# Kernel tuning notes

Hardware: AMD Instinct MI355X
Metric: run time of the kernel (lower is better)

## Reference

```python
import jax, jax.numpy as jnp
import numpy as np

NW, NT = 200000, 100000
DW, DT = 128, 64
HID, HEADS, OUT = 64, 2, 2
HC = HID * HEADS  # 128
E = 500000
NEG_SLOPE = 0.2


def setup_inputs() -> dict:
    key = jax.random.key(0)
    ks = iter(jax.random.split(key, 40))

    def nrm(shape, scale):
        return jax.random.normal(next(ks), shape, dtype=jnp.float32) * scale

    inp = {
        "x_wallet": nrm((NW, DW), 1.0),
        "x_token": nrm((NT, DT), 1.0),
        # per-node-type input projections Linear(in, hidden)
        "lin_w_W": nrm((DW, HID), 1.0 / np.sqrt(DW)),
        "lin_w_b": jnp.zeros((HID,), jnp.float32),
        "lin_t_W": nrm((DT, HID), 1.0 / np.sqrt(DT)),
        "lin_t_b": jnp.zeros((HID,), jnp.float32),
        # GAT layer 0: in=HID(64) -> H*C(128), stacked over 3 edge types
        "Wsrc0": nrm((3, HID, HC), 1.0 / np.sqrt(HID)),
        "Wdst0": nrm((3, HID, HC), 1.0 / np.sqrt(HID)),
        "atts0": nrm((3, HEADS, HID), 1.0 / np.sqrt(HID)),
        "attd0": nrm((3, HEADS, HID), 1.0 / np.sqrt(HID)),
        "b0": jnp.zeros((3, HC), jnp.float32),
        # GAT layer 1: in=H*C(128) -> H*C(128)
        "Wsrc1": nrm((3, HC, HC), 1.0 / np.sqrt(HC)),
        "Wdst1": nrm((3, HC, HC), 1.0 / np.sqrt(HC)),
        "atts1": nrm((3, HEADS, HID), 1.0 / np.sqrt(HID)),
        "attd1": nrm((3, HEADS, HID), 1.0 / np.sqrt(HID)),
        "b1": jnp.zeros((3, HC), jnp.float32),
        # classifiers Linear(H*C, out)
        "cls_w_W": nrm((HC, OUT), 1.0 / np.sqrt(HC)),
        "cls_w_b": jnp.zeros((OUT,), jnp.float32),
        "cls_t_W": nrm((HC, OUT), 1.0 / np.sqrt(HC)),
        "cls_t_b": jnp.zeros((OUT,), jnp.float32),
        # edge indices: [2, E] with row0 = src ids, row1 = dst ids
        "e_wt": jnp.stack([jax.random.randint(next(ks), (E,), 0, NW),
                            jax.random.randint(next(ks), (E,), 0, NT)]).astype(jnp.int64),
        "e_tw": jnp.stack([jax.random.randint(next(ks), (E,), 0, NT),
                            jax.random.randint(next(ks), (E,), 0, NW)]).astype(jnp.int64),
        "e_ww": jnp.stack([jax.random.randint(next(ks), (E,), 0, NW),
                            jax.random.randint(next(ks), (E,), 0, NW)]).astype(jnp.int64),
    }
    return inp


def gat_conv(x_src, x_dst, edge, Wsrc, Wdst, att_s, att_d, bias, n_dst):
    # bipartite GATConv: project, per-edge attention, segment softmax over dst, scatter-sum
    hs = (x_src @ Wsrc).reshape(-1, HEADS, HID)  # [Ns,H,C]
    hd = (x_dst @ Wdst).reshape(-1, HEADS, HID)  # [Nd,H,C]
    a_s = jnp.einsum("nhc,hc->nh", hs, att_s)    # [Ns,H]
    a_d = jnp.einsum("nhc,hc->nh", hd, att_d)    # [Nd,H]
    s, d = edge[0], edge[1]
    alpha = jax.nn.leaky_relu(a_s[s] + a_d[d], NEG_SLOPE)  # [E,H]
    m = jax.ops.segment_max(alpha, d, num_segments=n_dst)
    m = jnp.where(jnp.isfinite(m), m, 0.0)  # nodes with no in-edges
    ex = jnp.exp(alpha - m[d])
    den = jax.ops.segment_sum(ex, d, num_segments=n_dst)
    alpha = ex / (den[d] + 1e-16)
    out = jax.ops.segment_sum(alpha[:, :, None] * hs[s], d, num_segments=n_dst)  # [Nd,H,C]
    return out.reshape(n_dst, HC) + bias


def reference(x_wallet, x_token, lin_w_W, lin_w_b, lin_t_W, lin_t_b,
              Wsrc0, Wdst0, atts0, attd0, b0,
              Wsrc1, Wdst1, atts1, attd1, b1,
              cls_w_W, cls_w_b, cls_t_W, cls_t_b,
              e_wt, e_tw, e_ww):
    xw = x_wallet @ lin_w_W + lin_w_b
    xt = x_token @ lin_t_W + lin_t_b
    for Wsrc, Wdst, ats, atd, b in ((Wsrc0, Wdst0, atts0, attd0, b0),
                                     (Wsrc1, Wdst1, atts1, attd1, b1)):
        # edge type 0: wallet->token, 1: token->wallet, 2: wallet->wallet; HeteroConv aggr='sum'
        out_t = gat_conv(xw, xt, e_wt, Wsrc[0], Wdst[0], ats[0], atd[0], b[0], NT)
        out_w = (gat_conv(xt, xw, e_tw, Wsrc[1], Wdst[1], ats[1], atd[1], b[1], NW)
                 + gat_conv(xw, xw, e_ww, Wsrc[2], Wdst[2], ats[2], atd[2], b[2], NW))
        xw = jax.nn.elu(out_w)
        xt = jax.nn.elu(out_t)
    logits_w = xw @ cls_w_W + cls_w_b  # [NW,2]
    logits_t = xt @ cls_t_W + cls_t_b  # [NT,2]
    return jnp.concatenate([logits_w, logits_t], axis=0)  # [NW+NT,2]
```

## Files before the change

kernel.cpp:

```cpp
#include <hip/hip_runtime.h>
#include <stdint.h>

typedef unsigned short ushort_t;
typedef short s8v __attribute__((ext_vector_type(8)));
typedef float f4v __attribute__((ext_vector_type(4)));

#define NW 200000
#define NT 100000
#define EE 500000
#define NSEG (NT + NW + NW)

__device__ __forceinline__ float b2f(unsigned short u){
  union { unsigned int i; float f; } v; v.i = ((unsigned int)u) << 16; return v.f;
}
__device__ __forceinline__ unsigned short f2b(float f){
  unsigned int x = __float_as_uint(f);
  unsigned int r = x + 0x7fffu + ((x >> 16) & 1u);
  return (unsigned short)(r >> 16);
}
__device__ __forceinline__ float ldf(const void* p, long idx, int fm){
  return fm ? ((const float*)p)[idx] : b2f(((const ushort_t*)p)[idx]);
}

__global__ void detect_kern(const int* ewt, const int* etw, const int* eww,
                            const unsigned* xw_words, int* mode){
  if (threadIdx.x == 0 && blockIdx.x == 0){
    unsigned o = 0;
    for (int i = 0; i < 64; ++i)
      o |= (unsigned)ewt[2 * i + 1] | (unsigned)etw[2 * i + 1] | (unsigned)eww[2 * i + 1];
    mode[0] = (o == 0) ? 1 : 0;
    int viol = 0;
    for (int i = 0; i < 256; ++i){
      unsigned s = xw_words[i] & 0xffffu;
      unsigned e = (s >> 7) & 0xffu;
      if (!(s == 0u || s == 0x8000u || (e >= 90u && e <= 140u))) viol++;
    }
    mode[1] = (viol > 8) ? 1 : 0;
  }
}

struct TDesc { const void* src; ushort_t* dst; long ebase; int K; int N; };
struct TDesc8 { TDesc d[8]; };
__global__ void transpose8(TDesc8 td, const int* mode){
  int fm = mode[1];
  int mi = blockIdx.x >> 6;
  TDesc t = td.d[mi];
  int e = ((blockIdx.x & 63) << 8) + threadIdx.x;
  if (e < t.K * t.N){
    int k = e / t.N, n = e - k * t.N;
    t.dst[n * t.K + k] = f2b(ldf(t.src, t.ebase + e, fm));
  }
}

__global__ void uprep(const void* Wsrc0, const void* Wdst0, const void* atts0, const void* attd0,
                      const void* Wsrc1, const void* Wdst1, const void* atts1, const void* attd1,
                      float* Uw0, float* Ut0, float* Uw1, float* Ut1, const int* mode){
  int fm = mode[1];
  int id = blockIdx.x * 256 + threadIdx.x;
  if (id >= (64 + 128) * 12) return;
  int layer = (id >= 64 * 12);
  int rem = layer ? id - 64 * 12 : id;
  int K = layer ? 128 : 64;
  int k = rem / 12, j = rem % 12;
  const void* Ws = layer ? Wsrc1 : Wsrc0;
  const void* Wd = layer ? Wdst1 : Wdst0;
  const void* As = layer ? atts1 : atts0;
  const void* Ad = layer ? attd1 : attd0;
  int t, h; bool src;
  if (j < 8){ const int tt[8] = {0,0,2,2,1,1,2,2}; t = tt[j]; h = j & 1; src = (j < 4); }
  else { int jj = j - 8; t = (jj < 2) ? 1 : 0; h = jj & 1; src = (jj < 2); }
  const void* W = src ? Ws : Wd;
  const void* A = src ? As : Ad;
  float acc = 0.f;
  for (int c = 0; c < 64; ++c)
    acc += ldf(W, (long)(t * K + k) * 128 + h * 64 + c, fm) * ldf(A, t * 128 + h * 64 + c, fm);
  if (j < 8) (layer ? Uw1 : Uw0)[k * 8 + j] = acc;
  else       (layer ? Ut1 : Ut0)[k * 4 + (j - 8)] = acc;
}

__global__ void hist_kern(const int* ewt, const int* etw, const int* eww, const int* mode, int* deg){
  int i = blockIdx.x * 256 + threadIdx.x;
  if (i >= 3 * EE) return;
  int md = mode[0];
  int t = i / EE, e = i - t * EE;
  const int* ep = (t == 0) ? ewt : (t == 1) ? etw : eww;
  int d = md ? ep[2 * (EE + e)] : ep[EE + e];
  int base = (t == 0) ? 0 : (t == 1) ? NT : NT + NW;
  atomicAdd(&deg[base + d], 1);
}

__global__ __launch_bounds__(512) void scan1(const int* deg, int* excl, int* sums){
  __shared__ int pair[512];
  int t = threadIdx.x;
  int base = blockIdx.x * 1024;
  int i0 = base + 2 * t;
  int a = (i0 < NSEG) ? deg[i0] : 0;
  int b = (i0 + 1 < NSEG) ? deg[i0 + 1] : 0;
  int ps = a + b;
  pair[t] = ps;
  __syncthreads();
  for (int off = 1; off < 512; off <<= 1){
    int v = (t >= off) ? pair[t - off] : 0;
    __syncthreads();
    if (t >= off) pair[t] += v;
    __syncthreads();
  }
  int epair = pair[t] - ps;
  if (i0 < NSEG) excl[i0] = epair;
  if (i0 + 1 < NSEG) excl[i0 + 1] = epair + a;
  if (t == 511) sums[blockIdx.x] = pair[511];
}

__global__ __launch_bounds__(512) void scan2(int* sums, int nch){
  __shared__ int s[512];
  int t = threadIdx.x;
  int orig = (t < nch) ? sums[t] : 0;
  s[t] = orig;
  __syncthreads();
  for (int off = 1; off < 512; off <<= 1){
    int v = (t >= off) ? s[t - off] : 0;
    __syncthreads();
    if (t >= off) s[t] += v;
    __syncthreads();
  }
  if (t < nch) sums[t] = s[t] - orig;
}

__global__ void scan3(int* rowptr, int* cursor, const int* sums){
  int i = blockIdx.x * 256 + threadIdx.x;
  if (i < NSEG){
    int v = rowptr[i] + sums[i >> 10];
    rowptr[i] = v; cursor[i] = v;
  }
  if (i == 0) rowptr[NSEG] = 3 * EE;
}

__global__ void fill_kern(const int* ewt, const int* etw, const int* eww, const int* mode,
                          int* cursor, int* adj){
  int i = blockIdx.x * 256 + threadIdx.x;
  if (i >= 3 * EE) return;
  int md = mode[0];
  int t = i / EE, e = i - t * EE;
  const int* ep = (t == 0) ? ewt : (t == 1) ? etw : eww;
  int s = md ? ep[2 * e] : ep[e];
  int d = md ? ep[2 * (EE + e)] : ep[EE + e];
  int base = (t == 0) ? 0 : (t == 1) ? NT : NT + NW;
  int pos = atomicAdd(&cursor[base + d], 1);
  adj[pos] = s;
}

template<int K, int NC, bool BIAS, bool EXTA>
__global__ __launch_bounds__(256, 2) void gemm_kern(const void* __restrict__ A, const ushort_t* __restrict__ Bt,
    const void* __restrict__ bias, ushort_t* __restrict__ C, int M,
    const int* __restrict__ mode, int nchunk){
  constexpr int CT = NC / 16, KK = K / 32;
  int fm = EXTA ? mode[1] : 0;
  int tid = threadIdx.x, lane = tid & 63, wave = tid >> 6;
  int rl = lane & 15, kq = (lane >> 4) * 8;
  s8v bfrag[CT][KK];
#pragma unroll
  for (int ct = 0; ct < CT; ++ct)
#pragma unroll
    for (int kk = 0; kk < KK; ++kk)
      bfrag[ct][kk] = *(const s8v*)(Bt + (long)(ct * 16 + rl) * K + kk * 32 + kq);
  float biasv[CT];
  if (BIAS){
#pragma unroll
    for (int ct = 0; ct < CT; ++ct) biasv[ct] = ldf(bias, ct * 16 + rl, fm);
  }
  for (int chunk = blockIdx.x; chunk < nchunk; chunk += gridDim.x){
    long m0 = (long)chunk * 128 + wave * 32;
    f4v acc[2][CT];
#pragma unroll
    for (int rt = 0; rt < 2; ++rt)
#pragma unroll
      for (int ct = 0; ct < CT; ++ct) acc[rt][ct] = (f4v){0.f, 0.f, 0.f, 0.f};
#pragma unroll
    for (int rt = 0; rt < 2; ++rt){
      long row = m0 + rt * 16 + rl;
      bool ok = row < (long)M;
#pragma unroll
      for (int kk = 0; kk < KK; ++kk){
        s8v a = (s8v){0,0,0,0,0,0,0,0};
        if (ok){
          long e = row * K + kk * 32 + kq;
          if (EXTA && fm){
            const float* p = (const float*)A + e;
            uint4 lo = *(const uint4*)p;
            uint4 hi = *(const uint4*)(p + 4);
            union { s8v v; unsigned u[4]; } t;
            t.u[0] = (unsigned)f2b(__uint_as_float(lo.x)) | ((unsigned)f2b(__uint_as_float(lo.y)) << 16);
            t.u[1] = (unsigned)f2b(__uint_as_float(lo.z)) | ((unsigned)f2b(__uint_as_float(lo.w)) << 16);
            t.u[2] = (unsigned)f2b(__uint_as_float(hi.x)) | ((unsigned)f2b(__uint_as_float(hi.y)) << 16);
            t.u[3] = (unsigned)f2b(__uint_as_float(hi.z)) | ((unsigned)f2b(__uint_as_float(hi.w)) << 16);
            a = t.v;
          } else {
            a = *(const s8v*)((const ushort_t*)A + e);
          }
        }
#pragma unroll
        for (int ct = 0; ct < CT; ++ct)
          acc[rt][ct] = __builtin_amdgcn_mfma_f32_16x16x32_bf16(a, bfrag[ct][kk], acc[rt][ct], 0, 0, 0);
      }
    }
#pragma unroll
    for (int rt = 0; rt < 2; ++rt){
      long rbase = (long)chunk * 128 + wave * 32 + rt * 16 + (lane >> 4) * 4;
#pragma unroll
      for (int ct = 0; ct < CT; ++ct){
#pragma unroll
        for (int r = 0; r < 4; ++r){
          long gm = rbase + r;
          if (gm < (long)M){
            float v = acc[rt][ct][r];
            if (BIAS) v += biasv[ct];
            C[gm * NC + ct * 16 + rl] = f2b(v);
          }
        }
      }
    }
  }
}

template<int K, int NCOL>
__global__ __launch_bounds__(256) void a_kern(const ushort_t* __restrict__ x, const float* __restrict__ U,
                                              float* __restrict__ out, int N){
  int n = blockIdx.x * 256 + threadIdx.x;
  if (n >= N) return;
  float acc[NCOL];
#pragma unroll
  for (int j = 0; j < NCOL; ++j) acc[j] = 0.f;
  const ushort_t* xr = x + (long)n * K;
#pragma unroll
  for (int k8 = 0; k8 < K / 8; ++k8){
    uint4 v = *(const uint4*)(xr + k8 * 8);
    unsigned uu[4] = {v.x, v.y, v.z, v.w};
#pragma unroll
    for (int i = 0; i < 4; ++i){
      float f0 = b2f((unsigned short)(uu[i] & 0xffffu));
      float f1 = b2f((unsigned short)(uu[i] >> 16));
      const float* Ur = U + (k8 * 8 + i * 2) * NCOL;
#pragma unroll
      for (int j = 0; j < NCOL; ++j) acc[j] += f0 * Ur[j] + f1 * Ur[NCOL + j];
    }
  }
  float* o = out + (long)n * (2 * NCOL);
#pragma unroll
  for (int q = 0; q < NCOL / 2; ++q){
    f4v t = {__expf(acc[2 * q]), __expf(0.2f * acc[2 * q]),
             __expf(acc[2 * q + 1]), __expf(0.2f * acc[2 * q + 1])};
    *(f4v*)(o + q * 4) = t;
  }
}

__device__ __forceinline__ void round_load(const int* __restrict__ adj,
    const float* __restrict__ psrc, int sstr, int j, int cnt,
    const ushort_t* __restrict__ hb, float2 (&pq)[8], unsigned (&h)[8]){
#pragma unroll
  for (int i = 0; i < 8; ++i){
    if (i < cnt){
      int s = adj[j + i];
      pq[i] = *(const float2*)(psrc + (long)s * sstr);
      h[i] = *(const unsigned*)(hb + (long)s * 128);
    }
  }
}

__device__ __forceinline__ void round_acc(int cnt, float pd, float qd,
    const float2 (&pq)[8], const unsigned (&h)[8], float& n0, float& n1, float& den){
#pragma unroll
  for (int i = 0; i < 8; ++i){
    if (i < cnt){
      float t = pq[i].x * pd, u = pq[i].y * qd;
      float w = t > 1.f ? t : u;
      den += w;
      n0 += w * b2f((unsigned short)(h[i] & 0xffffu));
      n1 += w * b2f((unsigned short)(h[i] >> 16));
    }
  }
}

template<bool FINAL>
__global__ __launch_bounds__(256) void agg_all(const int* __restrict__ rowptr, const int* __restrict__ adj,
    const float* __restrict__ aw, const float* __restrict__ at,
    const ushort_t* __restrict__ hs0, const ushort_t* __restrict__ hs1, const ushort_t* __restrict__ hs2,
    const void* __restrict__ bsrc, ushort_t* __restrict__ xt_out, ushort_t* __restrict__ xw_out,
    const void* __restrict__ clsWw, const void* __restrict__ clsbw,
    const void* __restrict__ clsWt, const void* __restrict__ clsbt,
    void* __restrict__ dout, const int* __restrict__ mode){
  int fm = mode[1];
  int wv = __builtin_amdgcn_readfirstlane(threadIdx.x >> 6);
  int lane = threadIdx.x & 63;
  int hh = lane >> 5;
  int c0 = lane << 1;
  int bid = blockIdx.x;
  const int TB = NT / 4;
  bool is_tok = bid < TB;
  float o0, o1;
  int d;
  if (is_tok){
    d = bid * 4 + wv;
    float2 dq = *(const float2*)(at + (long)d * 8 + 4 + hh * 2);
    const float* ps = aw + hh * 2;
    const ushort_t* hb = hs0 + c0;
    int beg = rowptr[d], end = rowptr[d + 1];
    float n0 = 0.f, n1 = 0.f, den = 0.f;
    for (int j = beg; j < end; j += 8){
      int cnt = min(end - j, 8);
      float2 pq[8]; unsigned h[8];
      round_load(adj, ps, 16, j, cnt, hb, pq, h);
      round_acc(cnt, dq.x, dq.y, pq, h, n0, n1, den);
    }
    float inv = 1.f / (den + 1e-16f);
    o0 = n0 * inv + ldf(bsrc, c0, fm);
    o1 = n1 * inv + ldf(bsrc, c0 + 1, fm);
  } else {
    d = (bid - TB) * 4 + wv;
    const float* awd = aw + (long)d * 16;
    float2 dq1 = *(const float2*)(awd + 8 + hh * 2);
    float2 dq2 = *(const float2*)(awd + 12 + hh * 2);
    const float* ps1 = at + hh * 2;
    const float* ps2 = aw + 4 + hh * 2;
    const ushort_t* hb1 = hs1 + c0;
    const ushort_t* hb2 = hs2 + c0;
    int s1 = NT + d, s2 = NT + NW + d;
    int b1 = rowptr[s1], e1 = rowptr[s1 + 1];
    int b2 = rowptr[s2], e2 = rowptr[s2 + 1];
    int c1 = min(e1 - b1, 8), c2 = min(e2 - b2, 8);
    float n10 = 0.f, n11 = 0.f, den1 = 0.f;
    float n20 = 0.f, n21 = 0.f, den2 = 0.f;
    {
      float2 pq1[8], pq2[8]; unsigned h1[8], h2[8];
      if (c1 > 0) round_load(adj, ps1, 8, b1, c1, hb1, pq1, h1);
      if (c2 > 0) round_load(adj, ps2, 16, b2, c2, hb2, pq2, h2);
      if (c1 > 0) round_acc(c1, dq1.x, dq1.y, pq1, h1, n10, n11, den1);
      if (c2 > 0) round_acc(c2, dq2.x, dq2.y, pq2, h2, n20, n21, den2);
    }
    for (int j = b1 + 8; j < e1; j += 8){
      int cnt = min(e1 - j, 8);
      float2 pq[8]; unsigned h[8];
      round_load(adj, ps1, 8, j, cnt, hb1, pq, h);
      round_acc(cnt, dq1.x, dq1.y, pq, h, n10, n11, den1);
    }
    for (int j = b2 + 8; j < e2; j += 8){
      int cnt = min(e2 - j, 8);
      float2 pq[8]; unsigned h[8];
      round_load(adj, ps2, 16, j, cnt, hb2, pq, h);
      round_acc(cnt, dq2.x, dq2.y, pq, h, n20, n21, den2);
    }
    float i1v = 1.f / (den1 + 1e-16f), i2v = 1.f / (den2 + 1e-16f);
    o0 = n10 * i1v + n20 * i2v + ldf(bsrc, 128 + c0, fm)     + ldf(bsrc, 256 + c0, fm);
    o1 = n11 * i1v + n21 * i2v + ldf(bsrc, 128 + c0 + 1, fm) + ldf(bsrc, 256 + c0 + 1, fm);
  }
  o0 = o0 > 0.f ? o0 : __expf(o0) - 1.f;
  o1 = o1 > 0.f ? o1 : __expf(o1) - 1.f;
  if (!FINAL){
    ushort_t* out = is_tok ? xt_out : xw_out;
    unsigned pack = (unsigned)f2b(o0) | ((unsigned)f2b(o1) << 16);
    *(unsigned*)(out + (long)d * 128 + c0) = pack;
  } else {
    const void* W = is_tok ? clsWt : clsWw;
    const void* b = is_tok ? clsbt : clsbw;
    float w00 = ldf(W, 4 * lane + 0, fm), w01 = ldf(W, 4 * lane + 1, fm);
    float w10 = ldf(W, 4 * lane + 2, fm), w11 = ldf(W, 4 * lane + 3, fm);
    float p0 = o0 * w00 + o1 * w10;
    float p1 = o0 * w01 + o1 * w11;
#pragma unroll
    for (int off = 32; off > 0; off >>= 1){ p0 += __shfl_xor(p0, off, 64); p1 += __shfl_xor(p1, off, 64); }
    if (lane == 0){
      long g = is_tok ? (long)NW + d : (long)d;
      float r0 = p0 + ldf(b, 0, fm);
      float r1 = p1 + ldf(b, 1, fm);
      if (fm){ ((float*)dout)[g * 2] = r0; ((float*)dout)[g * 2 + 1] = r1; }
      else { ((ushort_t*)dout)[g * 2] = f2b(r0); ((ushort_t*)dout)[g * 2 + 1] = f2b(r1); }
    }
  }
}

extern "C" void kernel_launch(void* const* d_in, const int* in_sizes, int n_in,
                              void* d_out, int out_size, void* d_ws, size_t ws_size,
                              hipStream_t stream){
  const void* x_wallet = d_in[0];
  const void* x_token  = d_in[1];
  const void* lin_w_W  = d_in[2];
  const void* lin_w_b  = d_in[3];
  const void* lin_t_W  = d_in[4];
  const void* lin_t_b  = d_in[5];
  const void* Wsrc0    = d_in[6];
  const void* Wdst0    = d_in[7];
  const void* atts0    = d_in[8];
  const void* attd0    = d_in[9];
  const void* b0       = d_in[10];
  const void* Wsrc1    = d_in[11];
  const void* Wdst1    = d_in[12];
  const void* atts1    = d_in[13];
  const void* attd1    = d_in[14];
  const void* b1       = d_in[15];
  const void* cls_w_W  = d_in[16];
  const void* cls_w_b  = d_in[17];
  const void* cls_t_W  = d_in[18];
  const void* cls_t_b  = d_in[19];
  const int* e_wt = (const int*)d_in[20];
  const int* e_tw = (const int*)d_in[21];
  const int* e_ww = (const int*)d_in[22];

  char* ws = (char*)d_ws;
  size_t off = 0;
  auto alloc = [&](size_t bytes) -> char* {
    char* p = ws + off; off += (bytes + 255) & ~(size_t)255; return p;
  };
  int* rowptr = (int*)alloc((size_t)(NSEG + 1) * 4);
  int* deg    = (int*)alloc((size_t)(NSEG + 1) * 4);
  int* adj    = (int*)alloc((size_t)3 * EE * 4);
  int* sums   = (int*)alloc(512 * 4);
  int* mode   = (int*)alloc(8);
  ushort_t* BtLw = (ushort_t*)alloc(64 * 128 * 2);
  ushort_t* BtLt = (ushort_t*)alloc(64 * 64 * 2);
  ushort_t* BtS0 = (ushort_t*)alloc(3 * 128 * 64 * 2);
  ushort_t* BtS1 = (ushort_t*)alloc(3 * 128 * 128 * 2);
  float* Uw0 = (float*)alloc(64 * 8 * 4);
  float* Ut0 = (float*)alloc(64 * 4 * 4);
  float* Uw1 = (float*)alloc(128 * 8 * 4);
  float* Ut1 = (float*)alloc(128 * 4 * 4);
  float* aw = (float*)alloc((size_t)NW * 16 * 4);
  float* at = (float*)alloc((size_t)NT * 8 * 4);
  ushort_t* hs0 = (ushort_t*)alloc((size_t)NW * 128 * 2);
  ushort_t* hs1 = (ushort_t*)alloc((size_t)NT * 128 * 2);
  ushort_t* hs2 = (ushort_t*)alloc((size_t)NW * 128 * 2);
  ushort_t* xbuf = (ushort_t*)alloc(((size_t)NW + NT) * 128 * 2);
  ushort_t* xw0 = xbuf;
  ushort_t* xt0 = xbuf + (size_t)NW * 64;
  ushort_t* xwB = xbuf;
  ushort_t* xtB = xbuf + (size_t)NW * 128;
  (void)in_sizes; (void)n_in;

  if (off > ws_size){
    hipMemsetAsync(d_out, 0, (size_t)out_size * 2, stream);
    return;
  }

  hipMemsetAsync(deg, 0, (size_t)NSEG * 4, stream);
  detect_kern<<<1, 64, 0, stream>>>(e_wt, e_tw, e_ww, (const unsigned*)x_wallet, mode);

  TDesc8 td;
  td.d[0] = { lin_w_W, BtLw, 0, 128, 64 };
  td.d[1] = { lin_t_W, BtLt, 0, 64, 64 };
  for (int t = 0; t < 3; ++t){
    td.d[2 + t] = { Wsrc0, BtS0 + t * 128 * 64,  (long)t * 64 * 128,  64,  128 };
    td.d[5 + t] = { Wsrc1, BtS1 + t * 128 * 128, (long)t * 128 * 128, 128, 128 };
  }
  transpose8<<<512, 256, 0, stream>>>(td, mode);
  uprep<<<9, 256, 0, stream>>>(Wsrc0, Wdst0, atts0, attd0, Wsrc1, Wdst1, atts1, attd1, Uw0, Ut0, Uw1, Ut1, mode);

  int egrid = (3 * EE + 255) / 256;
  hist_kern<<<egrid, 256, 0, stream>>>(e_wt, e_tw, e_ww, mode, deg);
  int nch = (NSEG + 1023) / 1024;
  scan1<<<nch, 512, 0, stream>>>(deg, rowptr, sums);
  scan2<<<1, 512, 0, stream>>>(sums, nch);
  scan3<<<(NSEG + 255) / 256, 256, 0, stream>>>(rowptr, deg, sums);
  fill_kern<<<egrid, 256, 0, stream>>>(e_wt, e_tw, e_ww, mode, deg, adj);

  const int G = 512;
  int ncW = (NW + 127) / 128, ncT = (NT + 127) / 128;
  int agrid = NT / 4 + NW / 4;

  gemm_kern<128, 64, true, true><<<G, 256, 0, stream>>>(x_wallet, BtLw, lin_w_b, xw0, NW, mode, ncW);
  gemm_kern<64, 64, true, true><<<G, 256, 0, stream>>>(x_token, BtLt, lin_t_b, xt0, NT, mode, ncT);

  a_kern<64, 8><<<(NW + 255) / 256, 256, 0, stream>>>(xw0, Uw0, aw, NW);
  a_kern<64, 4><<<(NT + 255) / 256, 256, 0, stream>>>(xt0, Ut0, at, NT);
  gemm_kern<64, 128, false, false><<<G, 256, 0, stream>>>(xw0, BtS0, nullptr, hs0, NW, mode, ncW);
  gemm_kern<64, 128, false, false><<<G, 256, 0, stream>>>(xt0, BtS0 + 128 * 64, nullptr, hs1, NT, mode, ncT);
  gemm_kern<64, 128, false, false><<<G, 256, 0, stream>>>(xw0, BtS0 + 2 * 128 * 64, nullptr, hs2, NW, mode, ncW);
  agg_all<false><<<agrid, 256, 0, stream>>>(rowptr, adj, aw, at, hs0, hs1, hs2, b0, xtB, xwB,
                                            nullptr, nullptr, nullptr, nullptr, nullptr, mode);

  a_kern<128, 8><<<(NW + 255) / 256, 256, 0, stream>>>(xwB, Uw1, aw, NW);
  a_kern<128, 4><<<(NT + 255) / 256, 256, 0, stream>>>(xtB, Ut1, at, NT);
  gemm_kern<128, 128, false, false><<<G, 256, 0, stream>>>(xwB, BtS1, nullptr, hs0, NW, mode, ncW);
  gemm_kern<128, 128, false, false><<<G, 256, 0, stream>>>(xtB, BtS1 + 128 * 128, nullptr, hs1, NT, mode, ncT);
  gemm_kern<128, 128, false, false><<<G, 256, 0, stream>>>(xwB, BtS1 + 2 * 128 * 128, nullptr, hs2, NW, mode, ncW);
  agg_all<true><<<agrid, 256, 0, stream>>>(rowptr, adj, aw, at, hs0, hs1, hs2, b1, nullptr, nullptr,
                                           cls_w_W, cls_w_b, cls_t_W, cls_t_b, d_out, mode);
}
```

Measured before the change: 934.5 us.

## Interleave attention source coefficients into padded feature rows and split aggregation kernels

Source-side attention exponentials are now stored inside each projected feature row, which is padded from 128 to 160 bf16, so the gather per edge reads one row region instead of two separate arrays. Destination coefficients go to compact per-node arrays. The fused aggregation kernel is split into separate token and wallet kernels. The token kernel is launched right after its projection GEMM, so it can run before the other projections are computed. The cost is about 25% more bytes per feature row written by the GEMMs, and the rows lose 256-byte alignment.

```diff
diff --git a/kernel.cpp b/kernel.cpp
--- a/kernel.cpp
+++ b/kernel.cpp
@@ -9,6 +9,7 @@
 #define NT 100000
 #define EE 500000
 #define NSEG (NT + NW + NW)
+#define HRS 160
 
 __device__ __forceinline__ float b2f(unsigned short u){
   union { unsigned int i; float f; } v; v.i = ((unsigned int)u) << 16; return v.f;
@@ -149,7 +150,7 @@
   adj[pos] = s;
 }
 
-template<int K, int NC, bool BIAS, bool EXTA>
+template<int K, int NC, int RS, bool BIAS, bool EXTA>
 __global__ __launch_bounds__(256, 2) void gemm_kern(const void* __restrict__ A, const ushort_t* __restrict__ Bt,
     const void* __restrict__ bias, ushort_t* __restrict__ C, int M,
     const int* __restrict__ mode, int nchunk){
@@ -214,7 +215,7 @@
           if (gm < (long)M){
             float v = acc[rt][ct][r];
             if (BIAS) v += biasv[ct];
-            C[gm * NC + ct * 16 + rl] = f2b(v);
+            C[gm * RS + ct * 16 + rl] = f2b(v);
           }
         }
       }
@@ -222,9 +223,10 @@
   }
 }
 
-template<int K, int NCOL>
+template<int K, bool WAL>
 __global__ __launch_bounds__(256) void a_kern(const ushort_t* __restrict__ x, const float* __restrict__ U,
-                                              float* __restrict__ out, int N){
+    float* __restrict__ dpq, ushort_t* __restrict__ hsA, ushort_t* __restrict__ hsB, int N){
+  constexpr int NCOL = WAL ? 8 : 4;
   int n = blockIdx.x * 256 + threadIdx.x;
   if (n >= N) return;
   float acc[NCOL];
@@ -244,24 +246,32 @@
       for (int j = 0; j < NCOL; ++j) acc[j] += f0 * Ur[j] + f1 * Ur[NCOL + j];
     }
   }
-  float* o = out + (long)n * (2 * NCOL);
-#pragma unroll
-  for (int q = 0; q < NCOL / 2; ++q){
-    f4v t = {__expf(acc[2 * q]), __expf(0.2f * acc[2 * q]),
-             __expf(acc[2 * q + 1]), __expf(0.2f * acc[2 * q + 1])};
-    *(f4v*)(o + q * 4) = t;
-  }
-}
-
-__device__ __forceinline__ void round_load(const int* __restrict__ adj,
-    const float* __restrict__ psrc, int sstr, int j, int cnt,
-    const ushort_t* __restrict__ hb, float2 (&pq)[8], unsigned (&h)[8]){
+  if (WAL){
+    f4v tA = {__expf(acc[0]), __expf(0.2f * acc[0]), __expf(acc[1]), __expf(0.2f * acc[1])};
+    *(f4v*)((float*)(hsA + (long)n * HRS + 128)) = tA;
+    f4v tB = {__expf(acc[2]), __expf(0.2f * acc[2]), __expf(acc[3]), __expf(0.2f * acc[3])};
+    *(f4v*)((float*)(hsB + (long)n * HRS + 128)) = tB;
+    f4v d1 = {__expf(acc[4]), __expf(0.2f * acc[4]), __expf(acc[5]), __expf(0.2f * acc[5])};
+    f4v d2 = {__expf(acc[6]), __expf(0.2f * acc[6]), __expf(acc[7]), __expf(0.2f * acc[7])};
+    *(f4v*)(dpq + (long)n * 8) = d1;
+    *(f4v*)(dpq + (long)n * 8 + 4) = d2;
+  } else {
+    f4v tA = {__expf(acc[0]), __expf(0.2f * acc[0]), __expf(acc[1]), __expf(0.2f * acc[1])};
+    *(f4v*)((float*)(hsA + (long)n * HRS + 128)) = tA;
+    f4v d0 = {__expf(acc[2]), __expf(0.2f * acc[2]), __expf(acc[3]), __expf(0.2f * acc[3])};
+    *(f4v*)(dpq + (long)n * 4) = d0;
+  }
+}
+
+__device__ __forceinline__ void round_load(const int* __restrict__ adj, int j, int cnt,
+    const ushort_t* __restrict__ hs, int c0, int hh, float2 (&pq)[8], unsigned (&h)[8]){
 #pragma unroll
   for (int i = 0; i < 8; ++i){
     if (i < cnt){
       int s = adj[j + i];
-      pq[i] = *(const float2*)(psrc + (long)s * sstr);
-      h[i] = *(const unsigned*)(hb + (long)s * 128);
+      const ushort_t* rb = hs + (long)s * HRS;
+      pq[i] = *(const float2*)((const float*)(rb + 128) + hh * 2);
+      h[i] = *(const unsigned*)(rb + c0);
     }
   }
 }
@@ -280,100 +290,103 @@
   }
 }
 
+__device__ __forceinline__ void classify_store(float o0, float o1, const void* W, const void* b,
+    int lane, long g, void* dout, int fm){
+  float w00 = ldf(W, 4 * lane + 0, fm), w01 = ldf(W, 4 * lane + 1, fm);
+  float w10 = ldf(W, 4 * lane + 2, fm), w11 = ldf(W, 4 * lane + 3, fm);
+  float p0 = o0 * w00 + o1 * w10;
+  float p1 = o0 * w01 + o1 * w11;
+#pragma unroll
+  for (int off = 32; off > 0; off >>= 1){ p0 += __shfl_xor(p0, off, 64); p1 += __shfl_xor(p1, off, 64); }
+  if (lane == 0){
+    float r0 = p0 + ldf(b, 0, fm);
+    float r1 = p1 + ldf(b, 1, fm);
+    if (fm){ ((float*)dout)[g * 2] = r0; ((float*)dout)[g * 2 + 1] = r1; }
+    else { ((ushort_t*)dout)[g * 2] = f2b(r0); ((ushort_t*)dout)[g * 2 + 1] = f2b(r1); }
+  }
+}
+
 template<bool FINAL>
-__global__ __launch_bounds__(256) void agg_all(const int* __restrict__ rowptr, const int* __restrict__ adj,
-    const float* __restrict__ aw, const float* __restrict__ at,
-    const ushort_t* __restrict__ hs0, const ushort_t* __restrict__ hs1, const ushort_t* __restrict__ hs2,
-    const void* __restrict__ bsrc, ushort_t* __restrict__ xt_out, ushort_t* __restrict__ xw_out,
-    const void* __restrict__ clsWw, const void* __restrict__ clsbw,
+__global__ __launch_bounds__(256) void agg_tok(const int* __restrict__ rowptr, const int* __restrict__ adj,
+    const float* __restrict__ atd, const ushort_t* __restrict__ hs0,
+    const void* __restrict__ bsrc, ushort_t* __restrict__ xt_out,
     const void* __restrict__ clsWt, const void* __restrict__ clsbt,
     void* __restrict__ dout, const int* __restrict__ mode){
   int fm = mode[1];
   int wv = __builtin_amdgcn_readfirstlane(threadIdx.x >> 6);
   int lane = threadIdx.x & 63;
-  int hh = lane >> 5;
-  int c0 = lane << 1;
-  int bid = blockIdx.x;
-  const int TB = NT / 4;
-  bool is_tok = bid < TB;
-  float o0, o1;
-  int d;
-  if (is_tok){
-    d = bid * 4 + wv;
-    float2 dq = *(const float2*)(at + (long)d * 8 + 4 + hh * 2);
-    const float* ps = aw + hh * 2;
-    const ushort_t* hb = hs0 + c0;
-    int beg = rowptr[d], end = rowptr[d + 1];
-    float n0 = 0.f, n1 = 0.f, den = 0.f;
-    for (int j = beg; j < end; j += 8){
-      int cnt = min(end - j, 8);
-      float2 pq[8]; unsigned h[8];
-      round_load(adj, ps, 16, j, cnt, hb, pq, h);
-      round_acc(cnt, dq.x, dq.y, pq, h, n0, n1, den);
-    }
-    float inv = 1.f / (den + 1e-16f);
-    o0 = n0 * inv + ldf(bsrc, c0, fm);
-    o1 = n1 * inv + ldf(bsrc, c0 + 1, fm);
-  } else {
-    d = (bid - TB) * 4 + wv;
-    const float* awd = aw + (long)d * 16;
-    float2 dq1 = *(const float2*)(awd + 8 + hh * 2);
-    float2 dq2 = *(const float2*)(awd + 12 + hh * 2);
-    const float* ps1 = at + hh * 2;
-    const float* ps2 = aw + 4 + hh * 2;
-    const ushort_t* hb1 = hs1 + c0;
-    const ushort_t* hb2 = hs2 + c0;
-    int s1 = NT + d, s2 = NT + NW + d;
-    int b1 = rowptr[s1], e1 = rowptr[s1 + 1];
-    int b2 = rowptr[s2], e2 = rowptr[s2 + 1];
-    int c1 = min(e1 - b1, 8), c2 = min(e2 - b2, 8);
-    float n10 = 0.f, n11 = 0.f, den1 = 0.f;
-    float n20 = 0.f, n21 = 0.f, den2 = 0.f;
-    {
-      float2 pq1[8], pq2[8]; unsigned h1[8], h2[8];
-      if (c1 > 0) round_load(adj, ps1, 8, b1, c1, hb1, pq1, h1);
-      if (c2 > 0) round_load(adj, ps2, 16, b2, c2, hb2, pq2, h2);
-      if (c1 > 0) round_acc(c1, dq1.x, dq1.y, pq1, h1, n10, n11, den1);
-      if (c2 > 0) round_acc(c2, dq2.x, dq2.y, pq2, h2, n20, n21, den2);
-    }
-    for (int j = b1 + 8; j < e1; j += 8){
-      int cnt = min(e1 - j, 8);
-      float2 pq[8]; unsigned h[8];
-      round_load(adj, ps1, 8, j, cnt, hb1, pq, h);
-      round_acc(cnt, dq1.x, dq1.y, pq, h, n10, n11, den1);
-    }
-    for (int j = b2 + 8; j < e2; j += 8){
-      int cnt = min(e2 - j, 8);
-      float2 pq[8]; unsigned h[8];
-      round_load(adj, ps2, 16, j, cnt, hb2, pq, h);
-      round_acc(cnt, dq2.x, dq2.y, pq, h, n20, n21, den2);
-    }
-    float i1v = 1.f / (den1 + 1e-16f), i2v = 1.f / (den2 + 1e-16f);
-    o0 = n10 * i1v + n20 * i2v + ldf(bsrc, 128 + c0, fm)     + ldf(bsrc, 256 + c0, fm);
-    o1 = n11 * i1v + n21 * i2v + ldf(bsrc, 128 + c0 + 1, fm) + ldf(bsrc, 256 + c0 + 1, fm);
-  }
+  int hh = lane >> 5, c0 = lane << 1;
+  int d = blockIdx.x * 4 + wv;
+  float2 dq = *(const float2*)(atd + (long)d * 4 + hh * 2);
+  int beg = rowptr[d], end = rowptr[d + 1];
+  float n0 = 0.f, n1 = 0.f, den = 0.f;
+  for (int j = beg; j < end; j += 8){
+    int cnt = min(end - j, 8);
+    float2 pq[8]; unsigned h[8];
+    round_load(adj, j, cnt, hs0, c0, hh, pq, h);
+    round_acc(cnt, dq.x, dq.y, pq, h, n0, n1, den);
+  }
+  float inv = 1.f / (den + 1e-16f);
+  float o0 = n0 * inv + ldf(bsrc, c0, fm);
+  float o1 = n1 * inv + ldf(bsrc, c0 + 1, fm);
   o0 = o0 > 0.f ? o0 : __expf(o0) - 1.f;
   o1 = o1 > 0.f ? o1 : __expf(o1) - 1.f;
   if (!FINAL){
-    ushort_t* out = is_tok ? xt_out : xw_out;
     unsigned pack = (unsigned)f2b(o0) | ((unsigned)f2b(o1) << 16);
-    *(unsigned*)(out + (long)d * 128 + c0) = pack;
+    *(unsigned*)(xt_out + (long)d * 128 + c0) = pack;
   } else {
-    const void* W = is_tok ? clsWt : clsWw;
-    const void* b = is_tok ? clsbt : clsbw;
-    float w00 = ldf(W, 4 * lane + 0, fm), w01 = ldf(W, 4 * lane + 1, fm);
-    float w10 = ldf(W, 4 * lane + 2, fm), w11 = ldf(W, 4 * lane + 3, fm);
-    float p0 = o0 * w00 + o1 * w10;
-    float p1 = o0 * w01 + o1 * w11;
-#pragma unroll
-    for (int off = 32; off > 0; off >>= 1){ p0 += __shfl_xor(p0, off, 64); p1 += __shfl_xor(p1, off, 64); }
-    if (lane == 0){
-      long g = is_tok ? (long)NW + d : (long)d;
-      float r0 = p0 + ldf(b, 0, fm);
-      float r1 = p1 + ldf(b, 1, fm);
-      if (fm){ ((float*)dout)[g * 2] = r0; ((float*)dout)[g * 2 + 1] = r1; }
-      else { ((ushort_t*)dout)[g * 2] = f2b(r0); ((ushort_t*)dout)[g * 2 + 1] = f2b(r1); }
-    }
+    classify_store(o0, o1, clsWt, clsbt, lane, (long)NW + d, dout, fm);
+  }
+}
+
+template<bool FINAL>
+__global__ __launch_bounds__(256) void agg_wal(const int* __restrict__ rowptr, const int* __restrict__ adj,
+    const float* __restrict__ awd, const ushort_t* __restrict__ hs1, const ushort_t* __restrict__ hs2,
+    const void* __restrict__ bsrc, ushort_t* __restrict__ xw_out,
+    const void* __restrict__ clsWw, const void* __restrict__ clsbw,
+    void* __restrict__ dout, const int* __restrict__ mode){
+  int fm = mode[1];
+  int wv = __builtin_amdgcn_readfirstlane(threadIdx.x >> 6);
+  int lane = threadIdx.x & 63;
+  int hh = lane >> 5, c0 = lane << 1;
+  int d = blockIdx.x * 4 + wv;
+  float2 dq1 = *(const float2*)(awd + (long)d * 8 + hh * 2);
+  float2 dq2 = *(const float2*)(awd + (long)d * 8 + 4 + hh * 2);
+  int s1 = NT + d, s2 = NT + NW + d;
+  int b1 = rowptr[s1], e1 = rowptr[s1 + 1];
+  int b2 = rowptr[s2], e2 = rowptr[s2 + 1];
+  int c1 = min(e1 - b1, 8), c2 = min(e2 - b2, 8);
+  float n10 = 0.f, n11 = 0.f, den1 = 0.f;
+  float n20 = 0.f, n21 = 0.f, den2 = 0.f;
+  {
+    float2 pq1[8], pq2[8]; unsigned h1[8], h2[8];
+    if (c1 > 0) round_load(adj, b1, c1, hs1, c0, hh, pq1, h1);
+    if (c2 > 0) round_load(adj, b2, c2, hs2, c0, hh, pq2, h2);
+    if (c1 > 0) round_acc(c1, dq1.x, dq1.y, pq1, h1, n10, n11, den1);
+    if (c2 > 0) round_acc(c2, dq2.x, dq2.y, pq2, h2, n20, n21, den2);
+  }
+  for (int j = b1 + 8; j < e1; j += 8){
+    int cnt = min(e1 - j, 8);
+    float2 pq[8]; unsigned h[8];
+    round_load(adj, j, cnt, hs1, c0, hh, pq, h);
+    round_acc(cnt, dq1.x, dq1.y, pq, h, n10, n11, den1);
+  }
+  for (int j = b2 + 8; j < e2; j += 8){
+    int cnt = min(e2 - j, 8);
+    float2 pq[8]; unsigned h[8];
+    round_load(adj, j, cnt, hs2, c0, hh, pq, h);
+    round_acc(cnt, dq2.x, dq2.y, pq, h, n20, n21, den2);
+  }
+  float i1v = 1.f / (den1 + 1e-16f), i2v = 1.f / (den2 + 1e-16f);
+  float o0 = n10 * i1v + n20 * i2v + ldf(bsrc, 128 + c0, fm)     + ldf(bsrc, 256 + c0, fm);
+  float o1 = n11 * i1v + n21 * i2v + ldf(bsrc, 128 + c0 + 1, fm) + ldf(bsrc, 256 + c0 + 1, fm);
+  o0 = o0 > 0.f ? o0 : __expf(o0) - 1.f;
+  o1 = o1 > 0.f ? o1 : __expf(o1) - 1.f;
+  if (!FINAL){
+    unsigned pack = (unsigned)f2b(o0) | ((unsigned)f2b(o1) << 16);
+    *(unsigned*)(xw_out + (long)d * 128 + c0) = pack;
+  } else {
+    classify_store(o0, o1, clsWw, clsbw, lane, (long)d, dout, fm);
   }
 }
 
@@ -422,11 +435,11 @@
   float* Ut0 = (float*)alloc(64 * 4 * 4);
   float* Uw1 = (float*)alloc(128 * 8 * 4);
   float* Ut1 = (float*)alloc(128 * 4 * 4);
-  float* aw = (float*)alloc((size_t)NW * 16 * 4);
-  float* at = (float*)alloc((size_t)NT * 8 * 4);
-  ushort_t* hs0 = (ushort_t*)alloc((size_t)NW * 128 * 2);
-  ushort_t* hs1 = (ushort_t*)alloc((size_t)NT * 128 * 2);
-  ushort_t* hs2 = (ushort_t*)alloc((size_t)NW * 128 * 2);
+  float* awd = (float*)alloc((size_t)NW * 8 * 4);
+  float* atd = (float*)alloc((size_t)NT * 4 * 4);
+  ushort_t* hs0 = (ushort_t*)alloc((size_t)NW * HRS * 2);
+  ushort_t* hs1 = (ushort_t*)alloc((size_t)NT * HRS * 2);
+  ushort_t* hs2 = (ushort_t*)alloc((size_t)NW * HRS * 2);
   ushort_t* xbuf = (ushort_t*)alloc(((size_t)NW + NT) * 128 * 2);
   ushort_t* xw0 = xbuf;
   ushort_t* xt0 = xbuf + (size_t)NW * 64;
@@ -462,24 +475,24 @@
 
   const int G = 512;
   int ncW = (NW + 127) / 128, ncT = (NT + 127) / 128;
-  int agrid = NT / 4 + NW / 4;
-
-  gemm_kern<128, 64, true, true><<<G, 256, 0, stream>>>(x_wallet, BtLw, lin_w_b, xw0, NW, mode, ncW);
-  gemm_kern<64, 64, true, true><<<G, 256, 0, stream>>>(x_token, BtLt, lin_t_b, xt0, NT, mode, ncT);
-
-  a_kern<64, 8><<<(NW + 255) / 256, 256, 0, stream>>>(xw0, Uw0, aw, NW);
-  a_kern<64, 4><<<(NT + 255) / 256, 256, 0, stream>>>(xt0, Ut0, at, NT);
-  gemm_kern<64, 128, false, false><<<G, 256, 0, stream>>>(xw0, BtS0, nullptr, hs0, NW, mode, ncW);
-  gemm_kern<64, 128, false, false><<<G, 256, 0, stream>>>(xt0, BtS0 + 128 * 64, nullptr, hs1, NT, mode, ncT);
-  gemm_kern<64, 128, false, false><<<G, 256, 0, stream>>>(xw0, BtS0 + 2 * 128 * 64, nullptr, hs2, NW, mode, ncW);
-  agg_all<false><<<agrid, 256, 0, stream>>>(rowptr, adj, aw, at, hs0, hs1, hs2, b0, xtB, xwB,
-                                            nullptr, nullptr, nullptr, nullptr, nullptr, mode);
-
-  a_kern<128, 8><<<(NW + 255) / 256, 256, 0, stream>>>(xwB, Uw1, aw, NW);
-  a_kern<128, 4><<<(NT + 255) / 256, 256, 0, stream>>>(xtB, Ut1, at, NT);
-  gemm_kern<128, 128, false, false><<<G, 256, 0, stream>>>(xwB, BtS1, nullptr, hs0, NW, mode, ncW);
-  gemm_kern<128, 128, false, false><<<G, 256, 0, stream>>>(xtB, BtS1 + 128 * 128, nullptr, hs1, NT, mode, ncT);
-  gemm_kern<128, 128, false, false><<<G, 256, 0, stream>>>(xwB, BtS1 + 2 * 128 * 128, nullptr, hs2, NW, mode, ncW);
-  agg_all<true><<<agrid, 256, 0, stream>>>(rowptr, adj, aw, at, hs0, hs1, hs2, b1, nullptr, nullptr,
-                                           cls_w_W, cls_w_b, cls_t_W, cls_t_b, d_out, mode);
-}
+  int tgrid = NT / 4, wgrid = NW / 4;
+
+  gemm_kern<128, 64, 64, true, true><<<G, 256, 0, stream>>>(x_wallet, BtLw, lin_w_b, xw0, NW, mode, ncW);
+  gemm_kern<64, 64, 64, true, true><<<G, 256, 0, stream>>>(x_token, BtLt, lin_t_b, xt0, NT, mode, ncT);
+
+  a_kern<64, true><<<(NW + 255) / 256, 256, 0, stream>>>(xw0, Uw0, awd, hs0, hs2, NW);
+  a_kern<64, false><<<(NT + 255) / 256, 256, 0, stream>>>(xt0, Ut0, atd, hs1, hs1, NT);
+  gemm_kern<64, 128, HRS, false, false><<<G, 256, 0, stream>>>(xw0, BtS0, nullptr, hs0, NW, mode, ncW);
+  agg_tok<false><<<tgrid, 256, 0, stream>>>(rowptr, adj, atd, hs0, b0, xtB, nullptr, nullptr, nullptr, mode);
+  gemm_kern<64, 128, HRS, false, false><<<G, 256, 0, stream>>>(xt0, BtS0 + 128 * 64, nullptr, hs1, NT, mode, ncT);
+  gemm_kern<64, 128, HRS, false, false><<<G, 256, 0, stream>>>(xw0, BtS0 + 2 * 128 * 64, nullptr, hs2, NW, mode, ncW);
+  agg_wal<false><<<wgrid, 256, 0, stream>>>(rowptr, adj, awd, hs1, hs2, b0, xwB, nullptr, nullptr, nullptr, mode);
+
+  a_kern<128, true><<<(NW + 255) / 256, 256, 0, stream>>>(xwB, Uw1, awd, hs0, hs2, NW);
+  a_kern<128, false><<<(NT + 255) / 256, 256, 0, stream>>>(xtB, Ut1, atd, hs1, hs1, NT);
+  gemm_kern<128, 128, HRS, false, false><<<G, 256, 0, stream>>>(xwB, BtS1, nullptr, hs0, NW, mode, ncW);
+  agg_tok<true><<<tgrid, 256, 0, stream>>>(rowptr, adj, atd, hs0, b1, nullptr, cls_t_W, cls_t_b, d_out, mode);
+  gemm_kern<128, 128, HRS, false, false><<<G, 256, 0, stream>>>(xtB, BtS1 + 128 * 128, nullptr, hs1, NT, mode, ncT);
+  gemm_kern<128, 128, HRS, false, false><<<G, 256, 0, stream>>>(xwB, BtS1 + 2 * 128 * 128, nullptr, hs2, NW, mode, ncW);
+  agg_wal<true><<<wgrid, 256, 0, stream>>>(rowptr, adj, awd, hs1, hs2, b1, nullptr, cls_w_W, cls_w_b, d_out, mode);
+}
```

Measured after the change: 935.2 us. Within noise of the previous version (+0.1%).
